# Kernel tuning notes

Hardware: AMD Instinct MI355X
Metric: run time of the kernel (lower is better)

## Reference

```python
import jax, jax.numpy as jnp
import numpy as np

N_ENTS = 50000
N_RELS = 500
EMB = 256
N_LAYERS = 2
N_EDGES = 400000
BATCH = 512
BN_EPS = 1e-5


def make_quaternion_mul(kernel):
    # kernel: [m, 4*dim] -> hamilton: [4*m, 4*dim]
    r, i, j, k = jnp.split(kernel, 4, axis=1)
    r2 = jnp.concatenate([r, -i, -j, -k], axis=0)
    i2 = jnp.concatenate([i, r, -k, j], axis=0)
    j2 = jnp.concatenate([j, k, r, -i], axis=0)
    k2 = jnp.concatenate([k, -j, i, r], axis=0)
    return jnp.concatenate([r2, i2, j2, k2], axis=1)


def batchnorm(x, gamma, beta):
    mean = jnp.mean(x, axis=0)
    var = jnp.var(x, axis=0)  # biased, as torch BN training normalization
    return (x - mean) * jax.lax.rsqrt(var + BN_EPS) * gamma + beta


def q4gnn_layer(X, rows, cols, vals, W, gamma, beta, n_nodes):
    hamilton = make_quaternion_mul(W)          # [d, d]
    support = X @ hamilton                     # [n, d]
    agg = jax.ops.segment_sum(vals[:, None] * support[cols], rows, num_segments=n_nodes)
    return jnp.tanh(batchnorm(agg, gamma, beta))


def vec_vec_wise_multiplication(q, p):
    # quaternion componentwise-normalized hamilton product; q, p: [B, d]
    d = q.shape[1]
    size = d // 4
    pn = p.reshape(-1, 4, size)
    pn = pn / jnp.sqrt(jnp.sum(pn * pn, axis=1, keepdims=True))
    pn = pn.reshape(-1, d)
    qr, qi, qj, qk = jnp.split(q, 4, axis=1)
    q_r = jnp.concatenate([qr, -qi, -qj, -qk], axis=1)
    q_i = jnp.concatenate([qi, qr, -qk, qj], axis=1)
    q_j = jnp.concatenate([qj, qk, qr, -qi], axis=1)
    q_k = jnp.concatenate([qk, -qj, qi, qr], axis=1)
    def qwise(x):
        return jnp.sum((x * pn).reshape(-1, 4, size), axis=1)
    return jnp.concatenate([qwise(q_r), qwise(q_i), qwise(q_j), qwise(q_k)], axis=1)


def quate_score(h, r, X, gamma, beta):
    hr = vec_vec_wise_multiplication(h, r)
    hr = batchnorm(hr, gamma, beta)            # dropout = identity (eval)
    return hr @ X.T                            # [B, n_ents]


def setup_inputs() -> dict:
    key = jax.random.key(0)
    ks = jax.random.split(key, 12)
    return {
        "e1_idx": jax.random.randint(ks[0], (BATCH,), 0, N_ENTS),
        "r_idx": jax.random.randint(ks[1], (BATCH,), 0, N_RELS),
        "embeddings": jax.random.normal(ks[2], (N_ENTS + N_RELS, EMB), jnp.float32) * 0.1,
        "gcn1_w": jax.random.normal(ks[3], (N_LAYERS, EMB // 4, EMB), jnp.float32) * 0.1,
        "gcn2_w": jax.random.normal(ks[4], (N_LAYERS, EMB // 4, EMB), jnp.float32) * 0.1,
        "gcn1_gamma": jnp.ones((N_LAYERS, EMB), jnp.float32),
        "gcn1_beta": jnp.zeros((N_LAYERS, EMB), jnp.float32),
        "gcn2_gamma": jnp.ones((N_LAYERS, EMB), jnp.float32),
        "gcn2_beta": jnp.zeros((N_LAYERS, EMB), jnp.float32),
        "lin_ents": jax.random.normal(ks[5], (N_LAYERS, EMB // 2, EMB), jnp.float32) * 0.1,
        "bn_s_gamma": jnp.ones((3, EMB), jnp.float32),
        "bn_s_beta": jnp.zeros((3, EMB), jnp.float32),
        "adj_rows": jax.random.randint(ks[6], (N_EDGES,), 0, N_ENTS),
        "adj_cols": jax.random.randint(ks[7], (N_EDGES,), 0, N_ENTS),
        "adj_vals": jax.random.uniform(ks[8], (N_EDGES,), jnp.float32),
        "adjr_rows": jax.random.randint(ks[9], (N_EDGES,), 0, N_ENTS + N_RELS),
        "adjr_cols": jax.random.randint(ks[10], (N_EDGES,), 0, N_ENTS + N_RELS),
        "adjr_vals": jax.random.uniform(ks[11], (N_EDGES,), jnp.float32),
    }


def reference(e1_idx, r_idx, embeddings, gcn1_w, gcn2_w, gcn1_gamma, gcn1_beta,
              gcn2_gamma, gcn2_beta, lin_ents, bn_s_gamma, bn_s_beta,
              adj_rows, adj_cols, adj_vals, adjr_rows, adjr_cols, adjr_vals):
    X = embeddings[:N_ENTS]
    R = embeddings[N_ENTS:]
    scores = [jax.nn.sigmoid(quate_score(X[e1_idx], R[r_idx], X, bn_s_gamma[0], bn_s_beta[0]))]
    for l in range(N_LAYERS):
        XR = jnp.concatenate([X, R], axis=0)
        XRrf = q4gnn_layer(XR, adjr_rows, adjr_cols, adjr_vals,
                           gcn2_w[l], gcn2_gamma[l], gcn2_beta[l], N_ENTS + N_RELS)
        Xef = q4gnn_layer(X, adj_rows, adj_cols, adj_vals,
                          gcn1_w[l], gcn1_gamma[l], gcn1_beta[l], N_ENTS)
        Xrf = XRrf[:N_ENTS]
        # combine_type == 'cat': interleave quaternion components -> [N, 2*EMB]
        e1, e2, e3, e4 = jnp.split(Xef, 4, axis=1)
        r1, r2, r3, r4 = jnp.split(Xrf, 4, axis=1)
        Xcat = jnp.concatenate([e1, r1, e2, r2, e3, r3, e4, r4], axis=1)
        X = Xcat @ make_quaternion_mul(lin_ents[l])  # [N, EMB]
        R = XRrf[N_ENTS:]
        scores.append(jax.nn.sigmoid(
            quate_score(X[e1_idx], R[r_idx], X, bn_s_gamma[l + 1], bn_s_beta[l + 1])))
    return jnp.stack(scores)  # [N_LAYERS+1, B, N_ENTS]
```

## Files before the change

### kernel.cpp

```cpp
#include <hip/hip_runtime.h>
#include <math.h>

#define N_ENTS 50000
#define N_RELS 500
#define N_ALL  50500
#define EMB    256
#define NEDGE  400000
#define BATCH  512
#define BN_EPS 1e-5f

typedef unsigned short u16;
typedef unsigned int   u32;
typedef __attribute__((ext_vector_type(8))) short s16x8;
typedef __attribute__((ext_vector_type(4))) float f32x4;

#define LSTR 40

__device__ __forceinline__ u16 f2b(float x) {
    u32 u = __float_as_uint(x);
    return (u16)((u + 0x7fffu + ((u >> 16) & 1u)) >> 16);
}
__device__ __forceinline__ float b2f(u16 h) {
    return __uint_as_float((u32)h << 16);
}

__global__ __launch_bounds__(256) void split_kernel(
    const float* __restrict__ x, u16* __restrict__ hi, u16* __restrict__ lo,
    long n4) {
    long i = (long)blockIdx.x * 256 + threadIdx.x;
    if (i >= n4) return;
    float4 v = ((const float4*)x)[i];
    u16 h0 = f2b(v.x), h1 = f2b(v.y), h2 = f2b(v.z), h3 = f2b(v.w);
    u16 l0 = f2b(v.x - b2f(h0)), l1 = f2b(v.y - b2f(h1));
    u16 l2 = f2b(v.z - b2f(h2)), l3 = f2b(v.w - b2f(h3));
    uint2 hp, lp;
    hp.x = (u32)h0 | ((u32)h1 << 16); hp.y = (u32)h2 | ((u32)h3 << 16);
    lp.x = (u32)l0 | ((u32)l1 << 16); lp.y = (u32)l2 | ((u32)l3 << 16);
    ((uint2*)hi)[i] = hp;
    ((uint2*)lo)[i] = lp;
}

__global__ __launch_bounds__(256) void build_ht_kernel(
    const float* __restrict__ W, u16* __restrict__ Hhi, u16* __restrict__ Hlo,
    int P) {
    int K4 = 4 * P;
    int idx = blockIdx.x * 256 + threadIdx.x;
    int total = 256 * K4;
    if (idx >= total) return;
    int n = idx / K4, k = idx - n * K4;
    int a = k / P, p = k - a * P;
    int c = n >> 6, s = n & 63;
    const int  comp[4][4] = {{0,1,2,3},{1,0,3,2},{2,3,0,1},{3,2,1,0}};
    const float sgn[4][4] = {{1.f,1.f,1.f,1.f},
                             {-1.f,1.f,1.f,-1.f},
                             {-1.f,-1.f,1.f,1.f},
                             {-1.f,1.f,-1.f,1.f}};
    float v = sgn[a][c] * W[p * 256 + comp[a][c] * 64 + s];
    u16 h = f2b(v);
    Hhi[idx] = h;
    Hlo[idx] = f2b(v - b2f(h));
}

__device__ __forceinline__ void stage_split(
    const u16* __restrict__ Shi, const u16* __restrict__ Slo,
    long row0, int rows_left, int K, int k0,
    u16* __restrict__ Lh, u16* __restrict__ Ll, int tid) {
#pragma unroll
    for (int p = 0; p < 2; p++) {
        int idx = tid + p * 256;
        int r = idx >> 2, c = idx & 3;
        uint4 vh = make_uint4(0, 0, 0, 0), vl = make_uint4(0, 0, 0, 0);
        if (r < rows_left) {
            long base = (row0 + r) * (long)K + k0 + c * 8;
            vh = *(const uint4*)&Shi[base];
            vl = *(const uint4*)&Slo[base];
        }
        *(uint4*)&Lh[r * LSTR + c * 8] = vh;
        *(uint4*)&Ll[r * LSTR + c * 8] = vl;
    }
}

__device__ __forceinline__ void mfma_tile(
    const u16* __restrict__ Ah, const u16* __restrict__ Al,
    const u16* __restrict__ Bh, const u16* __restrict__ Bl,
    int wm, int wn, int lane, f32x4 acc[4][4]) {
    int lr = lane & 15, lkg = lane >> 4;
    s16x8 ah[4], al[4];
#pragma unroll
    for (int fm = 0; fm < 4; fm++) {
        int off = (wm + fm * 16 + lr) * LSTR + lkg * 8;
        ah[fm] = *(const s16x8*)&Ah[off];
        al[fm] = *(const s16x8*)&Al[off];
    }
#pragma unroll
    for (int fn = 0; fn < 4; fn++) {
        int off = (wn + fn * 16 + lr) * LSTR + lkg * 8;
        s16x8 bh = *(const s16x8*)&Bh[off];
        s16x8 bl = *(const s16x8*)&Bl[off];
#pragma unroll
        for (int fm = 0; fm < 4; fm++) {
            acc[fm][fn] = __builtin_amdgcn_mfma_f32_16x16x32_bf16(
                ah[fm], bh, acc[fm][fn], 0, 0, 0);
            acc[fm][fn] = __builtin_amdgcn_mfma_f32_16x16x32_bf16(
                ah[fm], bl, acc[fm][fn], 0, 0, 0);
            acc[fm][fn] = __builtin_amdgcn_mfma_f32_16x16x32_bf16(
                al[fm], bh, acc[fm][fn], 0, 0, 0);
        }
    }
}

__global__ __launch_bounds__(256) void mfma_gemm_bt_kernel(
    const u16* __restrict__ Ahi, const u16* __restrict__ Alo,
    const u16* __restrict__ Bhi, const u16* __restrict__ Blo,
    float* __restrict__ C, int M, int N, int K) {
    __shared__ u16 Ah[128 * LSTR], Al[128 * LSTR];
    __shared__ u16 Bh[128 * LSTR], Bl[128 * LSTR];
    int tid = threadIdx.x, lane = tid & 63, wid = tid >> 6;
    int wm = (wid >> 1) * 64, wn = (wid & 1) * 64;
    long bm0 = (long)blockIdx.y * 128, bn0 = (long)blockIdx.x * 128;
    int rA = (int)(((long)M - bm0 < 128) ? (long)M - bm0 : 128);
    int rB = (int)(((long)N - bn0 < 128) ? (long)N - bn0 : 128);
    f32x4 acc[4][4] = {};
    for (int k0 = 0; k0 < K; k0 += 32) {
        if (k0) __syncthreads();
        stage_split(Ahi, Alo, bm0, rA, K, k0, Ah, Al, tid);
        stage_split(Bhi, Blo, bn0, rB, K, k0, Bh, Bl, tid);
        __syncthreads();
        mfma_tile(Ah, Al, Bh, Bl, wm, wn, lane, acc);
    }
    int lr = lane & 15, lq = lane >> 4;
#pragma unroll
    for (int fm = 0; fm < 4; fm++) {
#pragma unroll
        for (int r = 0; r < 4; r++) {
            long row = bm0 + wm + fm * 16 + lq * 4 + r;
            if (row < M) {
#pragma unroll
                for (int fn = 0; fn < 4; fn++) {
                    long col = bn0 + wn + fn * 16 + lr;
                    if (col < N) C[row * N + col] = acc[fm][fn][r];
                }
            }
        }
    }
}

__global__ __launch_bounds__(256) void mfma_score_kernel(
    const u16* __restrict__ Ahi, const u16* __restrict__ Alo,
    const u16* __restrict__ Bhi, const u16* __restrict__ Blo,
    float* __restrict__ out) {
    __shared__ u16 Ah[128 * LSTR], Al[128 * LSTR];
    __shared__ u16 Bh[128 * LSTR], Bl[128 * LSTR];
    int tid = threadIdx.x, lane = tid & 63, wid = tid >> 6;
    int wm = (wid >> 1) * 64, wn = (wid & 1) * 64;
    long bm0 = (long)blockIdx.y * 128, bn0 = (long)blockIdx.x * 128;
    int rB = (int)(((long)N_ENTS - bn0 < 128) ? (long)N_ENTS - bn0 : 128);
    f32x4 acc[4][4] = {};
    for (int k0 = 0; k0 < 256; k0 += 32) {
        if (k0) __syncthreads();
        stage_split(Ahi, Alo, bm0, 128, 256, k0, Ah, Al, tid);
        stage_split(Bhi, Blo, bn0, rB, 256, k0, Bh, Bl, tid);
        __syncthreads();
        mfma_tile(Ah, Al, Bh, Bl, wm, wn, lane, acc);
    }
    int lr = lane & 15, lq = lane >> 4;
#pragma unroll
    for (int fm = 0; fm < 4; fm++) {
#pragma unroll
        for (int r = 0; r < 4; r++) {
            long row = bm0 + wm + fm * 16 + lq * 4 + r;
#pragma unroll
            for (int fn = 0; fn < 4; fn++) {
                long col = bn0 + wn + fn * 16 + lr;
                if (col < N_ENTS) {
                    float v = acc[fm][fn][r];
                    out[row * N_ENTS + col] = 1.f / (1.f + __expf(-v));
                }
            }
        }
    }
}

__device__ __forceinline__ float4 lin_a_load(const float* __restrict__ Xef,
                                             const float* __restrict__ Xrf,
                                             int gm, int kk, int M) {
    int chunk = kk >> 6, s = kk & 63;
    const float* src = (chunk & 1) ? Xrf : Xef;
    float4 v = make_float4(0.f, 0.f, 0.f, 0.f);
    if (gm < M) v = *(const float4*)&src[(long)gm * 256 + (chunk >> 1) * 64 + s];
    return v;
}

__global__ __launch_bounds__(256) void mfma_lin_kernel(
    const float* __restrict__ Xef, const float* __restrict__ Xrf,
    const u16* __restrict__ Bhi, const u16* __restrict__ Blo,
    float* __restrict__ C, int M) {
    __shared__ u16 Ah[128 * LSTR], Al[128 * LSTR];
    __shared__ u16 Bh[128 * LSTR], Bl[128 * LSTR];
    int tid = threadIdx.x, lane = tid & 63, wid = tid >> 6;
    int wm = (wid >> 1) * 64, wn = (wid & 1) * 64;
    int bm0 = blockIdx.y * 128;
    long bn0 = (long)blockIdx.x * 128;
    f32x4 acc[4][4] = {};
    for (int k0 = 0; k0 < 512; k0 += 32) {
        if (k0) __syncthreads();
#pragma unroll
        for (int p = 0; p < 4; p++) {
            int idx = tid + p * 256;
            int r = idx >> 3, c4 = idx & 7;
            float4 v = lin_a_load(Xef, Xrf, bm0 + r, k0 + c4 * 4, M);
            u16 h0 = f2b(v.x), h1 = f2b(v.y), h2 = f2b(v.z), h3 = f2b(v.w);
            u16 l0 = f2b(v.x - b2f(h0)), l1 = f2b(v.y - b2f(h1));
            u16 l2 = f2b(v.z - b2f(h2)), l3 = f2b(v.w - b2f(h3));
            uint2 hp, lp;
            hp.x = (u32)h0 | ((u32)h1 << 16); hp.y = (u32)h2 | ((u32)h3 << 16);
            lp.x = (u32)l0 | ((u32)l1 << 16); lp.y = (u32)l2 | ((u32)l3 << 16);
            *(uint2*)&Ah[r * LSTR + c4 * 4] = hp;
            *(uint2*)&Al[r * LSTR + c4 * 4] = lp;
        }
        stage_split(Bhi, Blo, bn0, 128, 512, k0, Bh, Bl, tid);
        __syncthreads();
        mfma_tile(Ah, Al, Bh, Bl, wm, wn, lane, acc);
    }
    int lr = lane & 15, lq = lane >> 4;
#pragma unroll
    for (int fm = 0; fm < 4; fm++) {
#pragma unroll
        for (int r = 0; r < 4; r++) {
            long row = (long)bm0 + wm + fm * 16 + lq * 4 + r;
            if (row < M) {
#pragma unroll
                for (int fn = 0; fn < 4; fn++) {
                    long col = bn0 + wn + fn * 16 + lr;
                    C[row * 256 + col] = acc[fm][fn][r];
                }
            }
        }
    }
}

__global__ __launch_bounds__(256) void hist_kernel(
    const int* __restrict__ rows, int* __restrict__ cnt, int n_edges) {
    int e = blockIdx.x * 256 + threadIdx.x;
    if (e < n_edges) atomicAdd(&cnt[rows[e]], 1);
}

__global__ __launch_bounds__(1024) void exscan_kernel(
    const int* __restrict__ cnt, int n, int* __restrict__ off) {
    __shared__ int part[1024];
    int t = threadIdx.x;
    int chunk = (n + 1023) / 1024;
    int lo = t * chunk;
    int hi = lo + chunk; if (hi > n) hi = n;
    int s = 0;
    for (int i = lo; i < hi; i++) s += cnt[i];
    part[t] = s;
    __syncthreads();
    for (int d = 1; d < 1024; d <<= 1) {
        int v = (t >= d) ? part[t - d] : 0;
        __syncthreads();
        part[t] += v;
        __syncthreads();
    }
    int base = (t == 0) ? 0 : part[t - 1];
    for (int i = lo; i < hi; i++) {
        off[i] = base;
        base += cnt[i];
    }
    if (hi >= n) off[n] = base;
}

__global__ __launch_bounds__(256) void scatter_kernel(
    const int* __restrict__ rows, const int* __restrict__ cols,
    const float* __restrict__ vals, int* __restrict__ cursor,
    int* __restrict__ csr_cols, float* __restrict__ csr_vals, int n_edges) {
    int e = blockIdx.x * 256 + threadIdx.x;
    if (e >= n_edges) return;
    int r = rows[e];
    int p = atomicAdd(&cursor[r], 1);
    csr_cols[p] = cols[e];
    csr_vals[p] = vals[e];
}

__global__ __launch_bounds__(256) void csr_agg_kernel(
    const float* __restrict__ support, const int* __restrict__ off,
    const int* __restrict__ ccols, const float* __restrict__ cvals,
    float* __restrict__ agg, int n_rows) {
    int gid = blockIdx.x * 256 + threadIdx.x;
    int row = gid >> 6;
    int lane = gid & 63;
    if (row >= n_rows) return;
    int beg = off[row], end = off[row + 1];
    float4 acc = {0.f, 0.f, 0.f, 0.f};
    for (int e = beg; e < end; e++) {
        int c = ccols[e];
        float v = cvals[e];
        const float4 s = *(const float4*)(support + (long)c * 256 + lane * 4);
        acc.x = fmaf(v, s.x, acc.x);
        acc.y = fmaf(v, s.y, acc.y);
        acc.z = fmaf(v, s.z, acc.z);
        acc.w = fmaf(v, s.w, acc.w);
    }
    *(float4*)(agg + (long)row * 256 + lane * 4) = acc;
}

__global__ __launch_bounds__(256) void bn_stats_kernel(
    const float* __restrict__ x, int n, float* __restrict__ stats) {
    int col = threadIdx.x;
    int r0 = blockIdx.x * 256;
    int r1 = r0 + 256;
    if (r1 > n) r1 = n;
    float s = 0.f, sq = 0.f;
    for (int r = r0; r < r1; r++) {
        float v = x[(long)r * 256 + col];
        s += v;
        sq += v * v;
    }
    atomicAdd(&stats[col], s);
    atomicAdd(&stats[256 + col], sq);
}

template <bool TANH>
__global__ __launch_bounds__(256) void bn_apply_kernel(
    const float* __restrict__ x, float* __restrict__ y, int n,
    const float* __restrict__ gamma, const float* __restrict__ beta,
    const float* __restrict__ stats) {
    long total = (long)n * 256;
    float inv_n = 1.f / (float)n;
    for (long idx = (long)blockIdx.x * 256 + threadIdx.x; idx < total;
         idx += (long)gridDim.x * 256) {
        int col = (int)(idx & 255);
        float mean = stats[col] * inv_n;
        float var = stats[256 + col] * inv_n - mean * mean;
        float sc = rsqrtf(var + BN_EPS) * gamma[col];
        float v = (x[idx] - mean) * sc + beta[col];
        if (TANH) v = tanhf(v);
        y[idx] = v;
    }
}

__global__ __launch_bounds__(256) void hr_kernel(
    const float* __restrict__ X, const float* __restrict__ R,
    const int* __restrict__ e1_idx, const int* __restrict__ r_idx,
    float* __restrict__ hr) {
    int idx = blockIdx.x * 256 + threadIdx.x;
    if (idx >= BATCH * 64) return;
    int b = idx >> 6, s = idx & 63;
    const float* h = X + (long)e1_idx[b] * 256;
    const float* p = R + (long)r_idx[b] * 256;
    float qr = h[s], qi = h[64 + s], qj = h[128 + s], qk = h[192 + s];
    float pr = p[s], pi = p[64 + s], pj = p[128 + s], pk = p[192 + s];
    float inv = rsqrtf(pr * pr + pi * pi + pj * pj + pk * pk);
    pr *= inv; pi *= inv; pj *= inv; pk *= inv;
    float* o = hr + (long)b * 256 + s;
    o[0]   = qr * pr - qi * pi - qj * pj - qk * pk;
    o[64]  = qi * pr + qr * pi - qk * pj + qj * pk;
    o[128] = qj * pr + qk * pi + qr * pj - qi * pk;
    o[192] = qk * pr - qj * pi + qi * pj + qr * pk;
}

struct Csr {
    int* off;
    int* cur;
    int* ccols;
    float* cvals;
};

struct Ws {
    float* supportBuf;
    float* aggA;
    float* aggB;
    float* XRcur;
    float* hr;
    float* hrn;
    float* stats;
    u16* xr_hi;
    u16* xr_lo;
    u16* hrn_hi;
    u16* hrn_lo;
    u16* ht_hi;
    u16* ht_lo;
    Csr adj;
    Csr adjr;
};

static void build_csr(const int* rows, const int* cols, const float* vals,
                      int n_rows, const Csr& c, hipStream_t stream) {
    hipMemsetAsync(c.cur, 0, (size_t)n_rows * sizeof(int), stream);
    hist_kernel<<<(NEDGE + 255) / 256, 256, 0, stream>>>(rows, c.cur, NEDGE);
    exscan_kernel<<<1, 1024, 0, stream>>>(c.cur, n_rows, c.off);
    hipMemcpyAsync(c.cur, c.off, (size_t)n_rows * sizeof(int),
                   hipMemcpyDeviceToDevice, stream);
    scatter_kernel<<<(NEDGE + 255) / 256, 256, 0, stream>>>(
        rows, cols, vals, c.cur, c.ccols, c.cvals, NEDGE);
}

static void run_bn(float* buf, float* outbuf, int n, const float* gamma,
                   const float* beta, bool do_tanh, const Ws& w,
                   hipStream_t stream) {
    hipMemsetAsync(w.stats, 0, 512 * sizeof(float), stream);
    bn_stats_kernel<<<(n + 255) / 256, 256, 0, stream>>>(buf, n, w.stats);
    long total = (long)n * 256;
    int blocks = (int)((total + 255) / 256);
    if (blocks > 2048) blocks = 2048;
    if (do_tanh)
        bn_apply_kernel<true><<<blocks, 256, 0, stream>>>(buf, outbuf, n, gamma, beta, w.stats);
    else
        bn_apply_kernel<false><<<blocks, 256, 0, stream>>>(buf, outbuf, n, gamma, beta, w.stats);
}

static void run_split(const float* x, u16* hi, u16* lo, long n,
                      hipStream_t stream) {
    long n4 = n / 4;
    split_kernel<<<(int)((n4 + 255) / 256), 256, 0, stream>>>(x, hi, lo, n4);
}

static void run_q4gnn(int n, const Csr& c, const float* W, const float* gamma,
                      const float* beta, float* agg, const Ws& w,
                      hipStream_t stream) {
    build_ht_kernel<<<(256 * 256) / 256, 256, 0, stream>>>(W, w.ht_hi, w.ht_lo, 64);
    dim3 g(2, (n + 127) / 128);
    mfma_gemm_bt_kernel<<<g, 256, 0, stream>>>(
        w.xr_hi, w.xr_lo, w.ht_hi, w.ht_lo, w.supportBuf, n, 256, 256);
    int agg_blocks = (n * 64 + 255) / 256;
    csr_agg_kernel<<<agg_blocks, 256, 0, stream>>>(
        w.supportBuf, c.off, c.ccols, c.cvals, agg, n);
    run_bn(agg, agg, n, gamma, beta, true, w, stream);
}

static void run_score(const float* X, const float* R, const int* e1_idx,
                      const int* r_idx, const float* gamma, const float* beta,
                      float* out_l, const Ws& w, hipStream_t stream) {
    hr_kernel<<<(BATCH * 64) / 256, 256, 0, stream>>>(X, R, e1_idx, r_idx, w.hr);
    run_bn(w.hr, w.hrn, BATCH, gamma, beta, false, w, stream);
    run_split(w.hrn, w.hrn_hi, w.hrn_lo, (long)BATCH * EMB, stream);
    dim3 g((N_ENTS + 127) / 128, BATCH / 128);
    mfma_score_kernel<<<g, 256, 0, stream>>>(
        w.hrn_hi, w.hrn_lo, w.xr_hi, w.xr_lo, out_l);
}

extern "C" void kernel_launch(void* const* d_in, const int* in_sizes, int n_in,
                              void* d_out, int out_size, void* d_ws, size_t ws_size,
                              hipStream_t stream) {
    const int*   e1_idx     = (const int*)d_in[0];
    const int*   r_idx      = (const int*)d_in[1];
    const float* emb        = (const float*)d_in[2];
    const float* gcn1_w     = (const float*)d_in[3];
    const float* gcn2_w     = (const float*)d_in[4];
    const float* gcn1_gamma = (const float*)d_in[5];
    const float* gcn1_beta  = (const float*)d_in[6];
    const float* gcn2_gamma = (const float*)d_in[7];
    const float* gcn2_beta  = (const float*)d_in[8];
    const float* lin_ents   = (const float*)d_in[9];
    const float* bn_s_gamma = (const float*)d_in[10];
    const float* bn_s_beta  = (const float*)d_in[11];
    const int*   adj_rows   = (const int*)d_in[12];
    const int*   adj_cols   = (const int*)d_in[13];
    const float* adj_vals   = (const float*)d_in[14];
    const int*   adjr_rows  = (const int*)d_in[15];
    const int*   adjr_cols  = (const int*)d_in[16];
    const float* adjr_vals  = (const float*)d_in[17];
    float* out = (float*)d_out;

    Ws w;
    float* f = (float*)d_ws;
    w.supportBuf = f; f += (long)N_ALL * EMB;
    w.aggA       = f; f += (long)N_ALL * EMB;
    w.aggB       = f; f += (long)N_ENTS * EMB;
    w.XRcur      = f; f += (long)N_ALL * EMB;
    w.hr         = f; f += BATCH * EMB;
    w.hrn        = f; f += BATCH * EMB;
    w.stats      = f; f += 512;
    w.xr_hi  = (u16*)f; f += (long)N_ALL * EMB / 2;
    w.xr_lo  = (u16*)f; f += (long)N_ALL * EMB / 2;
    w.hrn_hi = (u16*)f; f += BATCH * EMB / 2;
    w.hrn_lo = (u16*)f; f += BATCH * EMB / 2;
    w.ht_hi  = (u16*)f; f += 256 * 512 / 2;
    w.ht_lo  = (u16*)f; f += 256 * 512 / 2;
    int* ip = (int*)f;
    w.adj.off    = ip; ip += N_ENTS + 1;
    w.adj.cur    = ip; ip += N_ENTS;
    w.adj.ccols  = ip; ip += NEDGE;
    w.adjr.off   = ip; ip += N_ALL + 1;
    w.adjr.cur   = ip; ip += N_ALL;
    w.adjr.ccols = ip; ip += NEDGE;
    w.adj.cvals  = (float*)ip; ip += NEDGE;
    w.adjr.cvals = (float*)ip; ip += NEDGE;

    build_csr(adj_rows, adj_cols, adj_vals, N_ENTS, w.adj, stream);
    build_csr(adjr_rows, adjr_cols, adjr_vals, N_ALL, w.adjr, stream);

    run_split(emb, w.xr_hi, w.xr_lo, (long)N_ALL * EMB, stream);

    run_score(emb, emb + (long)N_ENTS * EMB, e1_idx, r_idx,
              bn_s_gamma, bn_s_beta, out, w, stream);

    for (int l = 0; l < 2; l++) {
        const float* XRptr = (l == 0) ? emb : w.XRcur;
        run_q4gnn(N_ALL, w.adjr, gcn2_w + (long)l * 64 * 256,
                  gcn2_gamma + l * 256, gcn2_beta + l * 256, w.aggA, w, stream);
        run_q4gnn(N_ENTS, w.adj, gcn1_w + (long)l * 64 * 256,
                  gcn1_gamma + l * 256, gcn1_beta + l * 256, w.aggB, w, stream);
        build_ht_kernel<<<(256 * 512) / 256, 256, 0, stream>>>(
            lin_ents + (long)l * 128 * 256, w.ht_hi, w.ht_lo, 128);
        dim3 g(2, (N_ENTS + 127) / 128);
        mfma_lin_kernel<<<g, 256, 0, stream>>>(
            w.aggB, w.aggA, w.ht_hi, w.ht_lo, w.XRcur, N_ENTS);
        hipMemcpyAsync(w.XRcur + (long)N_ENTS * EMB, w.aggA + (long)N_ENTS * EMB,
                       (size_t)N_RELS * EMB * sizeof(float),
                       hipMemcpyDeviceToDevice, stream);
        run_split(w.XRcur, w.xr_hi, w.xr_lo, (long)N_ALL * EMB, stream);
        run_score(w.XRcur, w.XRcur + (long)N_ENTS * EMB, e1_idx, r_idx,
                  bn_s_gamma + (l + 1) * 256, bn_s_beta + (l + 1) * 256,
                  out + (long)(l + 1) * BATCH * N_ENTS, w, stream);
        (void)XRptr;
    }
}
```

Before: 2.014 ms.

## Widen MFMA tiles to 128x256, fuse bf16 split into lin/BN, pack CSR

Each block now covers 128x256 of the output instead of 128x128, so the A operand is staged once per full N for the support, lin and score GEMMs, and the grid width is halved. The lin GEMM epilogue writes the hi/lo bf16 split directly, which removes the full-matrix split pass over entities. The score path fuses BN apply with the split. CSR columns and values are packed into int2 so each edge needs one load. The wider tiles double the accumulator registers (launch_bounds 256,2) and enlarge the B tile in LDS, which may reduce occupancy or cause spills.

```diff
diff --git a/kernel.cpp b/kernel.cpp
--- a/kernel.cpp
+++ b/kernel.cpp
@@ -61,12 +61,13 @@
     Hlo[idx] = f2b(v - b2f(h));
 }
 
-__device__ __forceinline__ void stage_split(
+template <int ROWS>
+__device__ __forceinline__ void stage_rows(
     const u16* __restrict__ Shi, const u16* __restrict__ Slo,
     long row0, int rows_left, int K, int k0,
     u16* __restrict__ Lh, u16* __restrict__ Ll, int tid) {
 #pragma unroll
-    for (int p = 0; p < 2; p++) {
+    for (int p = 0; p < ROWS / 64; p++) {
         int idx = tid + p * 256;
         int r = idx >> 2, c = idx & 3;
         uint4 vh = make_uint4(0, 0, 0, 0), vl = make_uint4(0, 0, 0, 0);
@@ -80,21 +81,21 @@
     }
 }
 
-__device__ __forceinline__ void mfma_tile(
+__device__ __forceinline__ void mfma_tile256(
     const u16* __restrict__ Ah, const u16* __restrict__ Al,
     const u16* __restrict__ Bh, const u16* __restrict__ Bl,
-    int wm, int wn, int lane, f32x4 acc[4][4]) {
-    int lr = lane & 15, lkg = lane >> 4;
+    int wm, int wn, int lane, f32x4 acc[4][8]) {
+    int lr = lane & 15, kg = lane >> 4;
     s16x8 ah[4], al[4];
 #pragma unroll
     for (int fm = 0; fm < 4; fm++) {
-        int off = (wm + fm * 16 + lr) * LSTR + lkg * 8;
+        int off = (wm + fm * 16 + lr) * LSTR + kg * 8;
         ah[fm] = *(const s16x8*)&Ah[off];
         al[fm] = *(const s16x8*)&Al[off];
     }
 #pragma unroll
-    for (int fn = 0; fn < 4; fn++) {
-        int off = (wn + fn * 16 + lr) * LSTR + lkg * 8;
+    for (int fn = 0; fn < 8; fn++) {
+        int off = (wn + fn * 16 + lr) * LSTR + kg * 8;
         s16x8 bh = *(const s16x8*)&Bh[off];
         s16x8 bl = *(const s16x8*)&Bl[off];
 #pragma unroll
@@ -109,24 +110,24 @@
     }
 }
 
-__global__ __launch_bounds__(256) void mfma_gemm_bt_kernel(
+__global__ __launch_bounds__(256, 2) void mfma_gemm_bt_kernel(
     const u16* __restrict__ Ahi, const u16* __restrict__ Alo,
     const u16* __restrict__ Bhi, const u16* __restrict__ Blo,
     float* __restrict__ C, int M, int N, int K) {
     __shared__ u16 Ah[128 * LSTR], Al[128 * LSTR];
-    __shared__ u16 Bh[128 * LSTR], Bl[128 * LSTR];
+    __shared__ u16 Bh[256 * LSTR], Bl[256 * LSTR];
     int tid = threadIdx.x, lane = tid & 63, wid = tid >> 6;
-    int wm = (wid >> 1) * 64, wn = (wid & 1) * 64;
-    long bm0 = (long)blockIdx.y * 128, bn0 = (long)blockIdx.x * 128;
+    int wm = (wid >> 1) * 64, wn = (wid & 1) * 128;
+    long bm0 = (long)blockIdx.y * 128, bn0 = (long)blockIdx.x * 256;
     int rA = (int)(((long)M - bm0 < 128) ? (long)M - bm0 : 128);
-    int rB = (int)(((long)N - bn0 < 128) ? (long)N - bn0 : 128);
-    f32x4 acc[4][4] = {};
+    int rB = (int)(((long)N - bn0 < 256) ? (long)N - bn0 : 256);
+    f32x4 acc[4][8] = {};
     for (int k0 = 0; k0 < K; k0 += 32) {
         if (k0) __syncthreads();
-        stage_split(Ahi, Alo, bm0, rA, K, k0, Ah, Al, tid);
-        stage_split(Bhi, Blo, bn0, rB, K, k0, Bh, Bl, tid);
+        stage_rows<128>(Ahi, Alo, bm0, rA, K, k0, Ah, Al, tid);
+        stage_rows<256>(Bhi, Blo, bn0, rB, K, k0, Bh, Bl, tid);
         __syncthreads();
-        mfma_tile(Ah, Al, Bh, Bl, wm, wn, lane, acc);
+        mfma_tile256(Ah, Al, Bh, Bl, wm, wn, lane, acc);
     }
     int lr = lane & 15, lq = lane >> 4;
 #pragma unroll
@@ -136,7 +137,7 @@
             long row = bm0 + wm + fm * 16 + lq * 4 + r;
             if (row < M) {
 #pragma unroll
-                for (int fn = 0; fn < 4; fn++) {
+                for (int fn = 0; fn < 8; fn++) {
                     long col = bn0 + wn + fn * 16 + lr;
                     if (col < N) C[row * N + col] = acc[fm][fn][r];
                 }
@@ -145,23 +146,23 @@
     }
 }
 
-__global__ __launch_bounds__(256) void mfma_score_kernel(
+__global__ __launch_bounds__(256, 2) void mfma_score_kernel(
     const u16* __restrict__ Ahi, const u16* __restrict__ Alo,
     const u16* __restrict__ Bhi, const u16* __restrict__ Blo,
     float* __restrict__ out) {
     __shared__ u16 Ah[128 * LSTR], Al[128 * LSTR];
-    __shared__ u16 Bh[128 * LSTR], Bl[128 * LSTR];
+    __shared__ u16 Bh[256 * LSTR], Bl[256 * LSTR];
     int tid = threadIdx.x, lane = tid & 63, wid = tid >> 6;
-    int wm = (wid >> 1) * 64, wn = (wid & 1) * 64;
-    long bm0 = (long)blockIdx.y * 128, bn0 = (long)blockIdx.x * 128;
-    int rB = (int)(((long)N_ENTS - bn0 < 128) ? (long)N_ENTS - bn0 : 128);
-    f32x4 acc[4][4] = {};
+    int wm = (wid >> 1) * 64, wn = (wid & 1) * 128;
+    long bm0 = (long)blockIdx.y * 128, bn0 = (long)blockIdx.x * 256;
+    int rB = (int)(((long)N_ENTS - bn0 < 256) ? (long)N_ENTS - bn0 : 256);
+    f32x4 acc[4][8] = {};
     for (int k0 = 0; k0 < 256; k0 += 32) {
         if (k0) __syncthreads();
-        stage_split(Ahi, Alo, bm0, 128, 256, k0, Ah, Al, tid);
-        stage_split(Bhi, Blo, bn0, rB, 256, k0, Bh, Bl, tid);
+        stage_rows<128>(Ahi, Alo, bm0, 128, 256, k0, Ah, Al, tid);
+        stage_rows<256>(Bhi, Blo, bn0, rB, 256, k0, Bh, Bl, tid);
         __syncthreads();
-        mfma_tile(Ah, Al, Bh, Bl, wm, wn, lane, acc);
+        mfma_tile256(Ah, Al, Bh, Bl, wm, wn, lane, acc);
     }
     int lr = lane & 15, lq = lane >> 4;
 #pragma unroll
@@ -170,7 +171,7 @@
         for (int r = 0; r < 4; r++) {
             long row = bm0 + wm + fm * 16 + lq * 4 + r;
 #pragma unroll
-            for (int fn = 0; fn < 4; fn++) {
+            for (int fn = 0; fn < 8; fn++) {
                 long col = bn0 + wn + fn * 16 + lr;
                 if (col < N_ENTS) {
                     float v = acc[fm][fn][r];
@@ -191,17 +192,17 @@
     return v;
 }
 
-__global__ __launch_bounds__(256) void mfma_lin_kernel(
+__global__ __launch_bounds__(256, 2) void mfma_lin_kernel(
     const float* __restrict__ Xef, const float* __restrict__ Xrf,
     const u16* __restrict__ Bhi, const u16* __restrict__ Blo,
-    float* __restrict__ C, int M) {
+    float* __restrict__ C, u16* __restrict__ Chi, u16* __restrict__ Clo,
+    int M) {
     __shared__ u16 Ah[128 * LSTR], Al[128 * LSTR];
-    __shared__ u16 Bh[128 * LSTR], Bl[128 * LSTR];
+    __shared__ u16 Bh[256 * LSTR], Bl[256 * LSTR];
     int tid = threadIdx.x, lane = tid & 63, wid = tid >> 6;
-    int wm = (wid >> 1) * 64, wn = (wid & 1) * 64;
+    int wm = (wid >> 1) * 64, wn = (wid & 1) * 128;
     int bm0 = blockIdx.y * 128;
-    long bn0 = (long)blockIdx.x * 128;
-    f32x4 acc[4][4] = {};
+    f32x4 acc[4][8] = {};
     for (int k0 = 0; k0 < 512; k0 += 32) {
         if (k0) __syncthreads();
 #pragma unroll
@@ -218,9 +219,9 @@
             *(uint2*)&Ah[r * LSTR + c4 * 4] = hp;
             *(uint2*)&Al[r * LSTR + c4 * 4] = lp;
         }
-        stage_split(Bhi, Blo, bn0, 128, 512, k0, Bh, Bl, tid);
+        stage_rows<256>(Bhi, Blo, 0, 256, 512, k0, Bh, Bl, tid);
         __syncthreads();
-        mfma_tile(Ah, Al, Bh, Bl, wm, wn, lane, acc);
+        mfma_tile256(Ah, Al, Bh, Bl, wm, wn, lane, acc);
     }
     int lr = lane & 15, lq = lane >> 4;
 #pragma unroll
@@ -230,9 +231,13 @@
             long row = (long)bm0 + wm + fm * 16 + lq * 4 + r;
             if (row < M) {
 #pragma unroll
-                for (int fn = 0; fn < 4; fn++) {
-                    long col = bn0 + wn + fn * 16 + lr;
-                    C[row * 256 + col] = acc[fm][fn][r];
+                for (int fn = 0; fn < 8; fn++) {
+                    long col = wn + fn * 16 + lr;
+                    float v = acc[fm][fn][r];
+                    C[row * 256 + col] = v;
+                    u16 h = f2b(v);
+                    Chi[row * 256 + col] = h;
+                    Clo[row * 256 + col] = f2b(v - b2f(h));
                 }
             }
         }
@@ -273,19 +278,17 @@
 __global__ __launch_bounds__(256) void scatter_kernel(
     const int* __restrict__ rows, const int* __restrict__ cols,
     const float* __restrict__ vals, int* __restrict__ cursor,
-    int* __restrict__ csr_cols, float* __restrict__ csr_vals, int n_edges) {
+    int2* __restrict__ pack, int n_edges) {
     int e = blockIdx.x * 256 + threadIdx.x;
     if (e >= n_edges) return;
     int r = rows[e];
     int p = atomicAdd(&cursor[r], 1);
-    csr_cols[p] = cols[e];
-    csr_vals[p] = vals[e];
+    pack[p] = make_int2(cols[e], __float_as_int(vals[e]));
 }
 
 __global__ __launch_bounds__(256) void csr_agg_kernel(
     const float* __restrict__ support, const int* __restrict__ off,
-    const int* __restrict__ ccols, const float* __restrict__ cvals,
-    float* __restrict__ agg, int n_rows) {
+    const int2* __restrict__ pack, float* __restrict__ agg, int n_rows) {
     int gid = blockIdx.x * 256 + threadIdx.x;
     int row = gid >> 6;
     int lane = gid & 63;
@@ -293,9 +296,9 @@
     int beg = off[row], end = off[row + 1];
     float4 acc = {0.f, 0.f, 0.f, 0.f};
     for (int e = beg; e < end; e++) {
-        int c = ccols[e];
-        float v = cvals[e];
-        const float4 s = *(const float4*)(support + (long)c * 256 + lane * 4);
+        int2 cv = pack[e];
+        float v = __int_as_float(cv.y);
+        const float4 s = *(const float4*)(support + (long)cv.x * 256 + lane * 4);
         acc.x = fmaf(v, s.x, acc.x);
         acc.y = fmaf(v, s.y, acc.y);
         acc.z = fmaf(v, s.z, acc.z);
@@ -337,6 +340,24 @@
         if (TANH) v = tanhf(v);
         y[idx] = v;
     }
+}
+
+__global__ __launch_bounds__(256) void bn_apply_split_kernel(
+    const float* __restrict__ x, u16* __restrict__ hi, u16* __restrict__ lo,
+    int n, const float* __restrict__ gamma, const float* __restrict__ beta,
+    const float* __restrict__ stats) {
+    long total = (long)n * 256;
+    float inv_n = 1.f / (float)n;
+    long idx = (long)blockIdx.x * 256 + threadIdx.x;
+    if (idx >= total) return;
+    int col = (int)(idx & 255);
+    float mean = stats[col] * inv_n;
+    float var = stats[256 + col] * inv_n - mean * mean;
+    float sc = rsqrtf(var + BN_EPS) * gamma[col];
+    float v = (x[idx] - mean) * sc + beta[col];
+    u16 h = f2b(v);
+    hi[idx] = h;
+    lo[idx] = f2b(v - b2f(h));
 }
 
 __global__ __launch_bounds__(256) void hr_kernel(
@@ -362,8 +383,7 @@
 struct Csr {
     int* off;
     int* cur;
-    int* ccols;
-    float* cvals;
+    int2* pack;
 };
 
 struct Ws {
@@ -372,7 +392,6 @@
     float* aggB;
     float* XRcur;
     float* hr;
-    float* hrn;
     float* stats;
     u16* xr_hi;
     u16* xr_lo;
@@ -392,7 +411,7 @@
     hipMemcpyAsync(c.cur, c.off, (size_t)n_rows * sizeof(int),
                    hipMemcpyDeviceToDevice, stream);
     scatter_kernel<<<(NEDGE + 255) / 256, 256, 0, stream>>>(
-        rows, cols, vals, c.cur, c.ccols, c.cvals, NEDGE);
+        rows, cols, vals, c.cur, c.pack, NEDGE);
 }
 
 static void run_bn(float* buf, float* outbuf, int n, const float* gamma,
@@ -419,12 +438,12 @@
                       const float* beta, float* agg, const Ws& w,
                       hipStream_t stream) {
     build_ht_kernel<<<(256 * 256) / 256, 256, 0, stream>>>(W, w.ht_hi, w.ht_lo, 64);
-    dim3 g(2, (n + 127) / 128);
+    dim3 g(1, (n + 127) / 128);
     mfma_gemm_bt_kernel<<<g, 256, 0, stream>>>(
         w.xr_hi, w.xr_lo, w.ht_hi, w.ht_lo, w.supportBuf, n, 256, 256);
     int agg_blocks = (n * 64 + 255) / 256;
     csr_agg_kernel<<<agg_blocks, 256, 0, stream>>>(
-        w.supportBuf, c.off, c.ccols, c.cvals, agg, n);
+        w.supportBuf, c.off, c.pack, agg, n);
     run_bn(agg, agg, n, gamma, beta, true, w, stream);
 }
 
@@ -432,9 +451,11 @@
                       const int* r_idx, const float* gamma, const float* beta,
                       float* out_l, const Ws& w, hipStream_t stream) {
     hr_kernel<<<(BATCH * 64) / 256, 256, 0, stream>>>(X, R, e1_idx, r_idx, w.hr);
-    run_bn(w.hr, w.hrn, BATCH, gamma, beta, false, w, stream);
-    run_split(w.hrn, w.hrn_hi, w.hrn_lo, (long)BATCH * EMB, stream);
-    dim3 g((N_ENTS + 127) / 128, BATCH / 128);
+    hipMemsetAsync(w.stats, 0, 512 * sizeof(float), stream);
+    bn_stats_kernel<<<(BATCH + 255) / 256, 256, 0, stream>>>(w.hr, BATCH, w.stats);
+    bn_apply_split_kernel<<<(BATCH * 256) / 256, 256, 0, stream>>>(
+        w.hr, w.hrn_hi, w.hrn_lo, BATCH, gamma, beta, w.stats);
+    dim3 g((N_ENTS + 255) / 256, BATCH / 128);
     mfma_score_kernel<<<g, 256, 0, stream>>>(
         w.hrn_hi, w.hrn_lo, w.xr_hi, w.xr_lo, out_l);
 }
@@ -469,7 +490,6 @@
     w.aggB       = f; f += (long)N_ENTS * EMB;
     w.XRcur      = f; f += (long)N_ALL * EMB;
     w.hr         = f; f += BATCH * EMB;
-    w.hrn        = f; f += BATCH * EMB;
     w.stats      = f; f += 512;
     w.xr_hi  = (u16*)f; f += (long)N_ALL * EMB / 2;
     w.xr_lo  = (u16*)f; f += (long)N_ALL * EMB / 2;
@@ -478,14 +498,12 @@
     w.ht_hi  = (u16*)f; f += 256 * 512 / 2;
     w.ht_lo  = (u16*)f; f += 256 * 512 / 2;
     int* ip = (int*)f;
+    w.adj.pack  = (int2*)ip; ip += 2 * NEDGE;
+    w.adjr.pack = (int2*)ip; ip += 2 * NEDGE;
     w.adj.off    = ip; ip += N_ENTS + 1;
     w.adj.cur    = ip; ip += N_ENTS;
-    w.adj.ccols  = ip; ip += NEDGE;
     w.adjr.off   = ip; ip += N_ALL + 1;
     w.adjr.cur   = ip; ip += N_ALL;
-    w.adjr.ccols = ip; ip += NEDGE;
-    w.adj.cvals  = (float*)ip; ip += NEDGE;
-    w.adjr.cvals = (float*)ip; ip += NEDGE;
 
     build_csr(adj_rows, adj_cols, adj_vals, N_ENTS, w.adj, stream);
     build_csr(adjr_rows, adjr_cols, adjr_vals, N_ALL, w.adjr, stream);
@@ -496,23 +514,22 @@
               bn_s_gamma, bn_s_beta, out, w, stream);
 
     for (int l = 0; l < 2; l++) {
-        const float* XRptr = (l == 0) ? emb : w.XRcur;
         run_q4gnn(N_ALL, w.adjr, gcn2_w + (long)l * 64 * 256,
                   gcn2_gamma + l * 256, gcn2_beta + l * 256, w.aggA, w, stream);
         run_q4gnn(N_ENTS, w.adj, gcn1_w + (long)l * 64 * 256,
                   gcn1_gamma + l * 256, gcn1_beta + l * 256, w.aggB, w, stream);
         build_ht_kernel<<<(256 * 512) / 256, 256, 0, stream>>>(
             lin_ents + (long)l * 128 * 256, w.ht_hi, w.ht_lo, 128);
-        dim3 g(2, (N_ENTS + 127) / 128);
+        dim3 g(1, (N_ENTS + 127) / 128);
         mfma_lin_kernel<<<g, 256, 0, stream>>>(
-            w.aggB, w.aggA, w.ht_hi, w.ht_lo, w.XRcur, N_ENTS);
+            w.aggB, w.aggA, w.ht_hi, w.ht_lo, w.XRcur, w.xr_hi, w.xr_lo, N_ENTS);
         hipMemcpyAsync(w.XRcur + (long)N_ENTS * EMB, w.aggA + (long)N_ENTS * EMB,
                        (size_t)N_RELS * EMB * sizeof(float),
                        hipMemcpyDeviceToDevice, stream);
-        run_split(w.XRcur, w.xr_hi, w.xr_lo, (long)N_ALL * EMB, stream);
+        run_split(w.XRcur + (long)N_ENTS * EMB, w.xr_hi + (long)N_ENTS * EMB,
+                  w.xr_lo + (long)N_ENTS * EMB, (long)N_RELS * EMB, stream);
         run_score(w.XRcur, w.XRcur + (long)N_ENTS * EMB, e1_idx, r_idx,
                   bn_s_gamma + (l + 1) * 256, bn_s_beta + (l + 1) * 256,
                   out + (long)(l + 1) * BATCH * N_ENTS, w, stream);
-        (void)XRptr;
-    }
-}
+    }
+}
```

Result: faster. 1.894 ms (-6.0%).
